# Performance work log

Measured on AMD Instinct MI355X. Metric: run time of the kernel, lower is better.

The kernel has to match this reference:

```python
import jax, jax.numpy as jnp
import numpy as np


def setup_inputs() -> dict:
    key = jax.random.key(0)
    k1, k2, k3 = jax.random.split(key, 3)
    N, K, QB = 8192, 8192, 128
    x = jax.random.normal(k1, (K,), dtype=jnp.float16)
    # packed int4 weights: two nibbles per byte, stored as int32 in [0, 256)
    packed_w = jax.random.randint(k2, (N, K // 2), 0, 256, dtype=jnp.int32)
    # per-(row, quant-block) FP16 scales, small positive values
    scales = (jax.random.uniform(k3, (N, K // QB), dtype=jnp.float32) * 0.05 + 0.001).astype(jnp.float16)
    return {"x": x, "packed_w": packed_w, "scales": scales, "qblock_size": QB}


def reference(x, packed_w, scales, qblock_size):
    # Unpack int4 weights: low nibble -> even k, high nibble -> odd k, offset-8.
    N, half_K = packed_w.shape
    K = half_K * 2
    lo = (packed_w & 0x0F) - 8          # [N, K/2]
    hi = ((packed_w >> 4) & 0x0F) - 8   # [N, K/2]
    w_int = jnp.stack([lo, hi], axis=-1).reshape(N, K).astype(jnp.float32)

    # Factored-scale GEMV (mirrors kernel: integer dot per quant-block, then one
    # multiply by the block scale).
    blocks = K // qblock_size
    wb = w_int.reshape(N, blocks, qblock_size)                 # [N, B, Q]
    xb = x.astype(jnp.float32).reshape(blocks, qblock_size)    # [B, Q]
    partial = jnp.einsum('nbq,bq->nb', wb, xb)                 # [N, B]
    out = jnp.sum(partial * scales.astype(jnp.float32), axis=1)
    return out.astype(jnp.float16)
```

## Files before the change

kernel.cpp:

```cpp
#include <hip/hip_runtime.h>


#define DEPTH 8

template<int ITERS>
__global__ __launch_bounds__(256, 4)
void eoq_gemv_pipe(const float* __restrict__ x,
                   const int* __restrict__ packed_w,
                   const float* __restrict__ scales,
                   float* __restrict__ out,
                   int N, int halfK, int sShift, int blocksPerRow)
{
    const int lane = threadIdx.x & 63;
    const int wave = threadIdx.x >> 6;
    const int row  = blockIdx.x * 4 + wave;
    if (row >= N) return;

    const int4*   __restrict__ w4p =
        reinterpret_cast<const int4*>(packed_w + (size_t)row * halfK);
    const float4* __restrict__ x4p = reinterpret_cast<const float4*>(x);
    const float*  __restrict__ srow = scales + (size_t)row * blocksPerRow;

    const float sAll = (lane < blocksPerRow) ? srow[lane] : 0.f;

    int4   wr[DEPTH];
    float4 xar[DEPTH];
    float4 xbr[DEPTH];

    #pragma unroll
    for (int p = 0; p < DEPTH; ++p) {
        const int j4 = (p << 6) + lane;
        wr[p]  = w4p[j4];
        xar[p] = x4p[2 * j4];
        xbr[p] = x4p[2 * j4 + 1];
    }

    float acc = 0.f;

    #pragma unroll
    for (int t = 0; t < ITERS; ++t) {
        const int slot = t & (DEPTH - 1);

        const int4   w4 = wr[slot];
        const float4 xa = xar[slot];
        const float4 xb = xbr[slot];

        if (t + DEPTH < ITERS) {
            const int j4 = ((t + DEPTH) << 6) + lane;
            wr[slot]  = w4p[j4];
            xar[slot] = x4p[2 * j4];
            xbr[slot] = x4p[2 * j4 + 1];
        }

        const float s = __shfl(sAll, ((t << 6) + lane) >> sShift, 64);

        const unsigned w0 = (unsigned)w4.x;
        const unsigned w1 = (unsigned)w4.y;
        const unsigned w2 = (unsigned)w4.z;
        const unsigned w3 = (unsigned)w4.w;

        float part = 0.f;
        part = fmaf((float)(int)(w0 & 0xFu) - 8.f, xa.x, part);
        part = fmaf((float)(int)(w0 >> 4)   - 8.f, xa.y, part);
        part = fmaf((float)(int)(w1 & 0xFu) - 8.f, xa.z, part);
        part = fmaf((float)(int)(w1 >> 4)   - 8.f, xa.w, part);
        part = fmaf((float)(int)(w2 & 0xFu) - 8.f, xb.x, part);
        part = fmaf((float)(int)(w2 >> 4)   - 8.f, xb.y, part);
        part = fmaf((float)(int)(w3 & 0xFu) - 8.f, xb.z, part);
        part = fmaf((float)(int)(w3 >> 4)   - 8.f, xb.w, part);
        acc = fmaf(s, part, acc);
    }

    #pragma unroll
    for (int off = 32; off > 0; off >>= 1)
        acc += __shfl_down(acc, off, 64);

    if (lane == 0) out[row] = acc;
}

__global__ __launch_bounds__(256, 2)
void eoq_gemv_generic(const float* __restrict__ x,
                      const int* __restrict__ packed_w,
                      const float* __restrict__ scales,
                      float* __restrict__ out,
                      int N, int halfK, int iters, int sShift, int blocksPerRow)
{
    const int lane = threadIdx.x & 63;
    const int wave = threadIdx.x >> 6;
    const int row  = blockIdx.x * 4 + wave;
    if (row >= N) return;

    const int4*   __restrict__ w4p =
        reinterpret_cast<const int4*>(packed_w + (size_t)row * halfK);
    const float4* __restrict__ x4p = reinterpret_cast<const float4*>(x);
    const float*  __restrict__ srow = scales + (size_t)row * blocksPerRow;

    float acc = 0.f;
    #pragma unroll 2
    for (int it = 0; it < iters; ++it) {
        const int j4 = (it << 6) + lane;
        const int4   w4 = w4p[j4];
        const float4 xa = x4p[2 * j4];
        const float4 xb = x4p[2 * j4 + 1];
        const float  s  = srow[j4 >> sShift];

        const unsigned w0 = (unsigned)w4.x;
        const unsigned w1 = (unsigned)w4.y;
        const unsigned w2 = (unsigned)w4.z;
        const unsigned w3 = (unsigned)w4.w;

        float part = 0.f;
        part = fmaf((float)(int)(w0 & 0xFu) - 8.f, xa.x, part);
        part = fmaf((float)(int)(w0 >> 4)   - 8.f, xa.y, part);
        part = fmaf((float)(int)(w1 & 0xFu) - 8.f, xa.z, part);
        part = fmaf((float)(int)(w1 >> 4)   - 8.f, xa.w, part);
        part = fmaf((float)(int)(w2 & 0xFu) - 8.f, xb.x, part);
        part = fmaf((float)(int)(w2 >> 4)   - 8.f, xb.y, part);
        part = fmaf((float)(int)(w3 & 0xFu) - 8.f, xb.z, part);
        part = fmaf((float)(int)(w3 >> 4)   - 8.f, xb.w, part);
        acc = fmaf(s, part, acc);
    }

    #pragma unroll
    for (int off = 32; off > 0; off >>= 1)
        acc += __shfl_down(acc, off, 64);

    if (lane == 0) out[row] = acc;
}

extern "C" void kernel_launch(void* const* d_in, const int* in_sizes, int n_in,
                              void* d_out, int out_size, void* d_ws, size_t ws_size,
                              hipStream_t stream) {
    const float* x      = (const float*)d_in[0];
    const int*   pw     = (const int*)d_in[1];
    const float* scales = (const float*)d_in[2];
    float*       out    = (float*)d_out;

    const int K     = in_sizes[0];
    const int halfK = K >> 1;
    const int N     = in_sizes[1] / halfK;
    const int blocksPerRow = in_sizes[2] / N;

    const int qhalf = halfK / blocksPerRow;
    int qhalfShift = 0;
    while ((1 << qhalfShift) < qhalf) ++qhalfShift;
    const int sShift = qhalfShift - 2;

    const int iters = halfK >> 8;

    dim3 grid((N + 3) / 4), block(256);
    if (iters == 16 && blocksPerRow <= 64) {
        eoq_gemv_pipe<16><<<grid, block, 0, stream>>>(
            x, pw, scales, out, N, halfK, sShift, blocksPerRow);
    } else {
        eoq_gemv_generic<<<grid, block, 0, stream>>>(
            x, pw, scales, out, N, halfK, iters, sShift, blocksPerRow);
    }
}
```

Measured before the change: 198.3 us.

## Sweep weight memory in flat chunk order with atomic row accumulation

Replaces the per-row pipelined kernel with a sweep kernel in which each wave handles 1KB chunks spread across the whole weight matrix (chunk index i*N+W), so concurrently running waves read a contiguous region of memory. Each chunk's partial dot product is reduced across the wave and added into the output row with an atomicAdd, after a memset zeroes the output. This aims to improve DRAM locality and streaming. In exchange it adds a per-chunk wave reduction, many atomics, an extra memset launch, drops the register prefetch pipeline, and makes the summation order nondeterministic.

```diff
diff --git a/kernel.cpp b/kernel.cpp
--- a/kernel.cpp
+++ b/kernel.cpp
@@ -1,58 +1,31 @@
 #include <hip/hip_runtime.h>
 
 
-#define DEPTH 8
-
-template<int ITERS>
 __global__ __launch_bounds__(256, 4)
-void eoq_gemv_pipe(const float* __restrict__ x,
-                   const int* __restrict__ packed_w,
-                   const float* __restrict__ scales,
-                   float* __restrict__ out,
-                   int N, int halfK, int sShift, int blocksPerRow)
+void eoq_gemv_sweep(const float* __restrict__ x,
+                    const int* __restrict__ packed_w,
+                    const float* __restrict__ scales,
+                    float* __restrict__ out,
+                    int N, int steps, int cpShift, int cpMask,
+                    int sShift, int blocksPerRow)
 {
     const int lane = threadIdx.x & 63;
-    const int wave = threadIdx.x >> 6;
-    const int row  = blockIdx.x * 4 + wave;
-    if (row >= N) return;
+    const int W    = blockIdx.x * 4 + (threadIdx.x >> 6);
 
-    const int4*   __restrict__ w4p =
-        reinterpret_cast<const int4*>(packed_w + (size_t)row * halfK);
-    const float4* __restrict__ x4p = reinterpret_cast<const float4*>(x);
-    const float*  __restrict__ srow = scales + (size_t)row * blocksPerRow;
+    const int4*   __restrict__ wflat = reinterpret_cast<const int4*>(packed_w);
+    const float4* __restrict__ x4p   = reinterpret_cast<const float4*>(x);
 
-    const float sAll = (lane < blocksPerRow) ? srow[lane] : 0.f;
+    #pragma unroll 4
+    for (int i = 0; i < steps; ++i) {
+        const int c   = i * N + W;
+        const int row = c >> cpShift;
+        const int pos = c & cpMask;
 
-    int4   wr[DEPTH];
-    float4 xar[DEPTH];
-    float4 xbr[DEPTH];
-
-    #pragma unroll
-    for (int p = 0; p < DEPTH; ++p) {
-        const int j4 = (p << 6) + lane;
-        wr[p]  = w4p[j4];
-        xar[p] = x4p[2 * j4];
-        xbr[p] = x4p[2 * j4 + 1];
-    }
-
-    float acc = 0.f;
-
-    #pragma unroll
-    for (int t = 0; t < ITERS; ++t) {
-        const int slot = t & (DEPTH - 1);
-
-        const int4   w4 = wr[slot];
-        const float4 xa = xar[slot];
-        const float4 xb = xbr[slot];
-
-        if (t + DEPTH < ITERS) {
-            const int j4 = ((t + DEPTH) << 6) + lane;
-            wr[slot]  = w4p[j4];
-            xar[slot] = x4p[2 * j4];
-            xbr[slot] = x4p[2 * j4 + 1];
-        }
-
-        const float s = __shfl(sAll, ((t << 6) + lane) >> sShift, 64);
+        const int4   w4 = wflat[(size_t)c * 64 + lane];
+        const float4 xa = x4p[(pos << 7) + (lane << 1)];
+        const float4 xb = x4p[(pos << 7) + (lane << 1) + 1];
+        const float  s  = scales[(size_t)row * blocksPerRow
+                                 + (((pos << 6) + lane) >> sShift)];
 
         const unsigned w0 = (unsigned)w4.x;
         const unsigned w1 = (unsigned)w4.y;
@@ -68,14 +41,14 @@
         part = fmaf((float)(int)(w2 >> 4)   - 8.f, xb.y, part);
         part = fmaf((float)(int)(w3 & 0xFu) - 8.f, xb.z, part);
         part = fmaf((float)(int)(w3 >> 4)   - 8.f, xb.w, part);
-        acc = fmaf(s, part, acc);
+
+        float v = part * s;
+        #pragma unroll
+        for (int off = 32; off > 0; off >>= 1)
+            v += __shfl_down(v, off, 64);
+
+        if (lane == 0) atomicAdd(&out[row], v);
     }
-
-    #pragma unroll
-    for (int off = 32; off > 0; off >>= 1)
-        acc += __shfl_down(acc, off, 64);
-
-    if (lane == 0) out[row] = acc;
 }
 
 __global__ __launch_bounds__(256, 2)
@@ -146,14 +119,25 @@
     while ((1 << qhalfShift) < qhalf) ++qhalfShift;
     const int sShift = qhalfShift - 2;
 
-    const int iters = halfK >> 8;
+    const int chunksPerRow = halfK >> 8;
+    int cpShift = 0;
+    while ((1 << cpShift) < chunksPerRow) ++cpShift;
 
-    dim3 grid((N + 3) / 4), block(256);
-    if (iters == 16 && blocksPerRow <= 64) {
-        eoq_gemv_pipe<16><<<grid, block, 0, stream>>>(
-            x, pw, scales, out, N, halfK, sShift, blocksPerRow);
+    const bool sweepOK =
+        (halfK % 256 == 0) &&
+        ((1 << cpShift) == chunksPerRow) &&
+        ((1 << qhalfShift) == qhalf) &&
+        (sShift >= 0) && (N % 4 == 0);
+
+    if (sweepOK) {
+        hipMemsetAsync(d_out, 0, (size_t)out_size * sizeof(float), stream);
+        dim3 grid(N / 4), block(256);
+        eoq_gemv_sweep<<<grid, block, 0, stream>>>(
+            x, pw, scales, out, N, chunksPerRow, cpShift, chunksPerRow - 1,
+            sShift, blocksPerRow);
     } else {
+        dim3 grid((N + 3) / 4), block(256);
         eoq_gemv_generic<<<grid, block, 0, stream>>>(
-            x, pw, scales, out, N, halfK, iters, sShift, blocksPerRow);
+            x, pw, scales, out, N, halfK, chunksPerRow, sShift, blocksPerRow);
     }
 }
```

Result: slower. 203.4 us (+2.6%).
